# Kernel tuning notes

Hardware: AMD Instinct MI355X
Metric: run time of the kernel (lower is better)

## Reference

```python
import jax, jax.numpy as jnp
import numpy as np

N = 50000      # total nodes in batched graph
E = 800000     # total edges
G = 512        # number of graphs in the batch
NF = 32        # input node feature dim
EF = 16        # edge feature dim
HID = [64, 128, 128, 256]


def _seg_mean(vals, ids, num):
    s = jax.ops.segment_sum(vals, ids, num_segments=num)
    c = jax.ops.segment_sum(jnp.ones((vals.shape[0], 1), vals.dtype), ids, num_segments=num)
    return s / jnp.maximum(c, 1.0)


def setup_inputs() -> dict:
    key = jax.random.key(0)
    ks = list(jax.random.split(key, 64))
    it = iter(ks)

    def nk():
        return next(it)

    inp = {}
    inp["x"] = jax.random.normal(nk(), (N, NF), jnp.float32)
    inp["e"] = jax.random.normal(nk(), (E, EF), jnp.float32)
    inp["src"] = jax.random.randint(nk(), (E,), 0, N)
    inp["dst"] = jax.random.randint(nk(), (E,), 0, N)
    inp["gid"] = jnp.sort(jax.random.randint(nk(), (N,), 0, G))
    fin = NF
    for i, f in enumerate(HID):
        inp[f"Wm{i}"] = jax.random.normal(nk(), (fin + EF, f), jnp.float32) / np.sqrt(fin + EF)
        inp[f"bm{i}"] = jnp.zeros((f,), jnp.float32)
        inp[f"Ws{i}"] = jax.random.normal(nk(), (fin, f), jnp.float32) / np.sqrt(fin)
        inp[f"bs{i}"] = jnp.zeros((f,), jnp.float32)
        inp[f"Wc{i}"] = jax.random.normal(nk(), (f, 1), jnp.float32) / np.sqrt(f)
        inp[f"bc{i}"] = jnp.zeros((1,), jnp.float32)
        fin = f
    return inp


def _molconv(x, e, src, dst, Wm, bm, Ws, bs):
    # gather source node feats, condition on edge feats, per-edge MLP
    m = jax.nn.relu(jnp.concatenate([x[src], e], axis=-1) @ Wm + bm)  # [E, out]
    agg = _seg_mean(m, dst, x.shape[0])                               # scatter-mean to dst
    return jax.nn.relu(agg + x @ Ws + bs)                             # [N, out]


def reference(x, e, src, dst, gid,
              Wm0, bm0, Ws0, bs0, Wc0, bc0,
              Wm1, bm1, Ws1, bs1, Wc1, bc1,
              Wm2, bm2, Ws2, bs2, Wc2, bc2,
              Wm3, bm3, Ws3, bs3, Wc3, bc3):
    layers = [(Wm0, bm0, Ws0, bs0, Wc0, bc0),
              (Wm1, bm1, Ws1, bs1, Wc1, bc1),
              (Wm2, bm2, Ws2, bs2, Wc2, bc2),
              (Wm3, bm3, Ws3, bs3, Wc3, bc3)]
    feat = x
    score = jnp.zeros((G, 1), x.dtype)
    for Wm, bm, Ws, bs, Wc, bc in layers:
        feat = _molconv(feat, e, src, dst, Wm, bm, Ws, bs)
        # per-layer Linear(feats,1) classifier + AvgPooling per graph, summed
        score = score + _seg_mean(feat @ Wc + bc, gid, G)
    return score
```

## Files before the change

kernel.cpp:

```cpp
#include <hip/hip_runtime.h>

#define NN 50000
#define EE 800000
#define GG 512
#define NP 50048
#define EB 3125
#define SCB 196

typedef short bf16x8 __attribute__((ext_vector_type(8)));
typedef float floatx4 __attribute__((ext_vector_type(4)));

__device__ inline unsigned short f2b(float f) {
    unsigned u = __float_as_uint(f);
    unsigned r = (u + 0x7fffu + ((u >> 16) & 1u)) >> 16;
    return (unsigned short)r;
}
__device__ inline float b2f(unsigned short b) {
    return __uint_as_float(((unsigned)b) << 16);
}


__global__ void conv_all(const float* __restrict__ x, unsigned short* __restrict__ xb, long n8x,
                         const float* __restrict__ ef, unsigned short* __restrict__ efB, long n8e) {
    long i = (long)blockIdx.x * blockDim.x + threadIdx.x;
    const float* s;
    unsigned short* d;
    long idx;
    if (i < n8x) { s = x; d = xb; idx = i; }
    else if (i < n8x + n8e) { s = ef; d = efB; idx = i - n8x; }
    else return;
    float4 a = ((const float4*)s)[2 * idx];
    float4 b = ((const float4*)s)[2 * idx + 1];
    unsigned short o[8] = {f2b(a.x), f2b(a.y), f2b(a.z), f2b(a.w),
                           f2b(b.x), f2b(b.y), f2b(b.z), f2b(b.w)};
    ((uint4*)d)[idx] = *(uint4*)o;
}


struct TpD { const float* W; unsigned short* WT; int K, F, Kp, rowOff; };
struct TpTab { TpD d[12]; };

__global__ void tp_all(TpTab t) {
    TpD dd = t.d[blockIdx.y];
    int f = blockIdx.x;
    if (f >= dd.F) return;
    for (int k = threadIdx.x; k < dd.Kp; k += blockDim.x)
        dd.WT[(size_t)f * dd.Kp + k] =
            (k < dd.K) ? f2b(dd.W[(size_t)(dd.rowOff + k) * dd.F + f]) : (unsigned short)0;
}


__global__ void hist_cnt(const int* __restrict__ dst, int* __restrict__ hist,
                         const int* __restrict__ gid, float* __restrict__ gcnt) {
    int b = blockIdx.x;
    if (b < EB) {
        int e = b * 256 + threadIdx.x;
        if (e < EE) atomicAdd(&hist[dst[e]], 1);
    } else {
        int n = (b - EB) * 256 + threadIdx.x;
        if (n < NN) atomicAdd(&gcnt[gid[n]], 1.0f);
    }
}

__global__ void scanA(const int* __restrict__ hist, int* __restrict__ bsum) {
    __shared__ int sb[256];
    int idx = blockIdx.x * 256 + threadIdx.x;
    sb[threadIdx.x] = (idx < NN) ? hist[idx] : 0;
    __syncthreads();
    for (int off = 128; off > 0; off >>= 1) {
        if (threadIdx.x < off) sb[threadIdx.x] += sb[threadIdx.x + off];
        __syncthreads();
    }
    if (threadIdx.x == 0) bsum[blockIdx.x] = sb[0];
}

__global__ void scanB(const int* __restrict__ bsum, int* __restrict__ boff) {
    __shared__ int sb[256];
    int t = threadIdx.x;
    int v = (t < SCB) ? bsum[t] : 0;
    sb[t] = v;
    __syncthreads();
    for (int off = 1; off < 256; off <<= 1) {
        int u = (t >= off) ? sb[t - off] : 0;
        __syncthreads();
        sb[t] += u;
        __syncthreads();
    }
    if (t < SCB) boff[t] = sb[t] - v;
}

__global__ void scanC(const int* __restrict__ hist, const int* __restrict__ boff,
                      int* __restrict__ cursor, float* __restrict__ invdeg,
                      float* __restrict__ gcnt, float* __restrict__ score,
                      const float* __restrict__ bc0, const float* __restrict__ bc1,
                      const float* __restrict__ bc2, const float* __restrict__ bc3) {
    __shared__ int sb[256];
    int t = threadIdx.x;
    int idx = blockIdx.x * 256 + t;
    int v = (idx < NN) ? hist[idx] : 0;
    sb[t] = v;
    __syncthreads();
    for (int off = 1; off < 256; off <<= 1) {
        int u = (t >= off) ? sb[t - off] : 0;
        __syncthreads();
        sb[t] += u;
        __syncthreads();
    }
    if (idx < NN) {
        cursor[idx] = boff[blockIdx.x] + sb[t] - v;
        invdeg[idx] = 1.0f / fmaxf((float)v, 1.0f);
    }
    if (idx < GG) {
        float c = gcnt[idx];
        gcnt[idx] = 1.0f / fmaxf(c, 1.0f);
        score[idx] = (c > 0.0f) ? (bc0[0] + bc1[0] + bc2[0] + bc3[0]) : 0.0f;
    }
}

__global__ void scatter_kernel(const int* __restrict__ src, const int* __restrict__ dst,
                               int* __restrict__ cursor, const unsigned short* __restrict__ efB,
                               int* __restrict__ srcS, int* __restrict__ dstS,
                               unsigned short* __restrict__ efS) {
    int e = blockIdx.x * blockDim.x + threadIdx.x;
    if (e < EE) {
        int d = dst[e];
        int p = atomicAdd(&cursor[d], 1);
        srcS[p] = src[e];
        dstS[p] = d;
        const uint4* s = (const uint4*)&efB[(size_t)e * 16];
        uint4* dd = (uint4*)&efS[(size_t)p * 16];
        dd[0] = s[0];
        dd[1] = s[1];
    }
}


template<int FIN, int F>
__global__ __launch_bounds__(256)
void nodeP(const unsigned short* __restrict__ featB, const unsigned short* __restrict__ WxT,
           unsigned short* __restrict__ P, float* __restrict__ agg)
{
    const int tid = threadIdx.x;
    const int w   = tid >> 6;
    const int l   = tid & 63;
    const int l16 = l & 15;
    const int q   = l >> 4;
    const int cb  = blockIdx.y * 64;
    const int nb  = blockIdx.x * 64;
    const int row = nb + w * 16 + l16;

    {
        const int zr = nb + (tid >> 4);
        const int zc = cb + ((tid & 15) << 2);
        const float4 z4 = {0.f, 0.f, 0.f, 0.f};
        #pragma unroll
        for (int i = 0; i < 4; ++i) {
            int n = zr + i * 16;
            if (n < NN) *(float4*)&agg[(size_t)n * F + zc] = z4;
        }
    }

    floatx4 acc[4];
    #pragma unroll
    for (int nt = 0; nt < 4; ++nt) acc[nt] = (floatx4){0.f, 0.f, 0.f, 0.f};

    #pragma unroll
    for (int kb = 0; kb < FIN; kb += 32) {
        bf16x8 a = *(const bf16x8*)&featB[(size_t)row * FIN + kb + q * 8];
        #pragma unroll
        for (int nt = 0; nt < 4; ++nt) {
            bf16x8 b = *(const bf16x8*)&WxT[(size_t)(cb + nt * 16 + l16) * FIN + kb + q * 8];
            acc[nt] = __builtin_amdgcn_mfma_f32_16x16x32_bf16(a, b, acc[nt], 0, 0, 0);
        }
    }

    #pragma unroll
    for (int nt = 0; nt < 4; ++nt)
        #pragma unroll
        for (int r = 0; r < 4; ++r) {
            int ro = nb + w * 16 + q * 4 + r;
            P[(size_t)ro * F + cb + nt * 16 + l16] = f2b(acc[nt][r]);
        }
}


#define RXO(r) ((((r) >> 2 & 1) << 4) | (((r) >> 3 & 1) << 3))

template<int F>
__global__ __launch_bounds__(256)
void edge_q(const unsigned short* __restrict__ efS,
            const int* __restrict__ srcS, const int* __restrict__ dstS,
            const unsigned short* __restrict__ WeT, const unsigned short* __restrict__ P,
            const float* __restrict__ bm, float* __restrict__ agg)
{
    constexpr int CW  = (F >= 128) ? 128 : 64;
    constexpr int WPG = F / CW;
    constexpr int NT  = CW / 16;
    constexpr int EPB = 64 * (4 / WPG);
    constexpr int RS  = CW;

    __shared__ __align__(16) float red[4][16 * RS];

    const int tid = threadIdx.x;
    const int w   = tid >> 6;
    const int l   = tid & 63;
    const int l16 = l & 15;
    const int q   = l >> 4;
    const int sub = w / WPG;
    const int cb  = (w % WPG) * CW;
    const int be  = blockIdx.x * EPB + sub * 64;

    const int dreg = dstS[be + l];
    const int sreg = srcS[be + l];

    const int dnext = __shfl_down(dreg, 1);
    const unsigned long long em = __ballot((l == 63) || (dreg != dnext));

    const bf16x8 ZV = {0, 0, 0, 0, 0, 0, 0, 0};
    const int xo = ((q & 1) << 4) | ((q >> 1) << 3);
    float* redw = &red[w][0];

    bf16x8 bfr[NT];
    #pragma unroll
    for (int nt = 0; nt < NT; ++nt)
        bfr[nt] = *(const bf16x8*)&WeT[(size_t)(cb + nt * 16 + l16) * 32 + q * 8];

    if constexpr (CW == 128) {
        float2 bmv;
        bmv.x = bm[cb + 2 * l];
        bmv.y = bm[cb + 2 * l + 1];

        float2 csum = {0.f, 0.f};
        bool first = true;

        #pragma unroll
        for (int mt = 0; mt < 4; ++mt) {
            bf16x8 a = ZV;
            if (q < 2) a = *(const bf16x8*)&efS[(size_t)(be + mt * 16 + l16) * 16 + q * 8];
            unsigned pvv[16];
            #pragma unroll
            for (int r = 0; r < 16; ++r) {
                int sr = __shfl(sreg, mt * 16 + r);
                pvv[r] = *(const unsigned*)&P[(size_t)sr * F + cb + 2 * l];
            }

            #pragma unroll
            for (int nt = 0; nt < NT; ++nt) {
                floatx4 acc = __builtin_amdgcn_mfma_f32_16x16x32_bf16(
                    a, bfr[nt], (floatx4){0.f, 0.f, 0.f, 0.f}, 0, 0, 0);
                #pragma unroll
                for (int r4 = 0; r4 < 4; ++r4)
                    redw[(q * 4 + r4) * RS + ((nt * 16 + l16) ^ xo)] = acc[r4];
            }

            #pragma unroll
            for (int r = 0; r < 16; ++r) {
                const int gr = mt * 16 + r;
                float2 qv = *(const float2*)&redw[r * RS + ((2 * l) ^ RXO(r))];
                csum.x += fmaxf(qv.x + __uint_as_float(pvv[r] << 16)          + bmv.x, 0.f);
                csum.y += fmaxf(qv.y + __uint_as_float(pvv[r] & 0xffff0000u) + bmv.y, 0.f);
                if ((em >> gr) & 1ull) {
                    int d = __shfl(dreg, gr);
                    float* ap = &agg[(size_t)d * F + cb + 2 * l];
                    if (first || gr == 63) { atomicAdd(ap, csum.x); atomicAdd(ap + 1, csum.y); }
                    else                   { *(float2*)ap = csum; }
                    csum.x = 0.f; csum.y = 0.f;
                    first = false;
                }
            }
        }
    } else {
        const float bmv = bm[cb + l];

        float csum = 0.f;
        bool first = true;

        #pragma unroll
        for (int mt = 0; mt < 4; ++mt) {
            bf16x8 a = ZV;
            if (q < 2) a = *(const bf16x8*)&efS[(size_t)(be + mt * 16 + l16) * 16 + q * 8];
            float pvv[16];
            #pragma unroll
            for (int r = 0; r < 16; ++r) {
                int sr = __shfl(sreg, mt * 16 + r);
                pvv[r] = b2f(P[(size_t)sr * F + cb + l]);
            }

            #pragma unroll
            for (int nt = 0; nt < NT; ++nt) {
                floatx4 acc = __builtin_amdgcn_mfma_f32_16x16x32_bf16(
                    a, bfr[nt], (floatx4){0.f, 0.f, 0.f, 0.f}, 0, 0, 0);
                #pragma unroll
                for (int r4 = 0; r4 < 4; ++r4)
                    redw[(q * 4 + r4) * RS + ((nt * 16 + l16) ^ xo)] = acc[r4];
            }

            #pragma unroll
            for (int r = 0; r < 16; ++r) {
                const int gr = mt * 16 + r;
                float qv = redw[r * RS + (l ^ RXO(r))];
                csum += fmaxf(qv + pvv[r] + bmv, 0.f);
                if ((em >> gr) & 1ull) {
                    int d = __shfl(dreg, gr);
                    float* ap = &agg[(size_t)d * F + cb + l];
                    if (first || gr == 63) atomicAdd(ap, csum);
                    else                   *ap = csum;
                    csum = 0.f;
                    first = false;
                }
            }
        }
    }
}


template<int FIN, int F>
__global__ __launch_bounds__(256)
void node_mfma(const unsigned short* __restrict__ featB, const float* __restrict__ agg,
               const unsigned short* __restrict__ WsT, const float* __restrict__ bs,
               const float* __restrict__ Wc, const float* __restrict__ invdeg,
               unsigned short* __restrict__ fout, float* __restrict__ rd)
{
    const int tid = threadIdx.x;
    const int w   = tid >> 6;
    const int l   = tid & 63;
    const int l16 = l & 15;
    const int q   = l >> 4;
    const int cb  = blockIdx.y * 64;
    const int nb  = blockIdx.x * 64;
    const int row = nb + w * 16 + l16;

    floatx4 acc[4];
    #pragma unroll
    for (int nt = 0; nt < 4; ++nt) acc[nt] = (floatx4){0.f, 0.f, 0.f, 0.f};

    #pragma unroll
    for (int kb = 0; kb < FIN; kb += 32) {
        bf16x8 a = *(const bf16x8*)&featB[(size_t)row * FIN + kb + q * 8];
        #pragma unroll
        for (int nt = 0; nt < 4; ++nt) {
            bf16x8 b = *(const bf16x8*)&WsT[(size_t)(cb + nt * 16 + l16) * FIN + kb + q * 8];
            acc[nt] = __builtin_amdgcn_mfma_f32_16x16x32_bf16(a, b, acc[nt], 0, 0, 0);
        }
    }

    float wcv[4], bsv[4];
    #pragma unroll
    for (int nt = 0; nt < 4; ++nt) {
        wcv[nt] = Wc[cb + nt * 16 + l16];
        bsv[nt] = bs[cb + nt * 16 + l16];
    }

    #pragma unroll
    for (int r = 0; r < 4; ++r) {
        int n = nb + w * 16 + q * 4 + r;
        bool valid = n < NN;
        float idg = valid ? invdeg[n] : 0.f;
        float s = 0.f;
        #pragma unroll
        for (int nt = 0; nt < 4; ++nt) {
            int col = cb + nt * 16 + l16;
            float av = valid ? agg[(size_t)n * F + col] : 0.f;
            float v = fmaxf(acc[nt][r] + av * idg + bsv[nt], 0.f);
            if (valid) fout[(size_t)n * F + col] = f2b(v);
            s += v * wcv[nt];
        }
        s += __shfl_xor(s, 1);
        s += __shfl_xor(s, 2);
        s += __shfl_xor(s, 4);
        s += __shfl_xor(s, 8);
        if (valid && l16 == 0) atomicAdd(&rd[n], s);
    }
}


__global__ void score_reduce(const float* __restrict__ rd, const int* __restrict__ gid,
                             const float* __restrict__ invg, float* __restrict__ score) {
    int n = blockIdx.x * blockDim.x + threadIdx.x;
    int l = threadIdx.x & 63;
    bool valid = n < NN;
    int g = valid ? gid[n] : -1;
    float v = valid ? rd[n] : 0.f;
    #pragma unroll
    for (int off = 1; off < 64; off <<= 1) {
        float vo = __shfl_up(v, off);
        int go = __shfl_up(g, off);
        if (l >= off && go == g) v += vo;
    }
    int gn = __shfl_down(g, 1);
    bool tail = (l == 63) || (gn != g);
    if (valid && tail) atomicAdd(&score[g], v * invg[g]);
}


extern "C" void kernel_launch(void* const* d_in, const int* in_sizes, int n_in,
                              void* d_out, int out_size, void* d_ws, size_t ws_size,
                              hipStream_t stream) {
    const float* x   = (const float*)d_in[0];
    const float* ef  = (const float*)d_in[1];
    const int*   src = (const int*)d_in[2];
    const int*   dst = (const int*)d_in[3];
    const int*   gid = (const int*)d_in[4];
    const float *Wm[4], *bm[4], *Ws[4], *bs[4], *Wc[4], *bc[4];
    for (int i = 0; i < 4; ++i) {
        Wm[i] = (const float*)d_in[5 + 6 * i];
        bm[i] = (const float*)d_in[6 + 6 * i];
        Ws[i] = (const float*)d_in[7 + 6 * i];
        bs[i] = (const float*)d_in[8 + 6 * i];
        Wc[i] = (const float*)d_in[9 + 6 * i];
        bc[i] = (const float*)d_in[10 + 6 * i];
    }

    char* w = (char*)d_ws;
    float* agg = (float*)w;                  w += (size_t)NN * 256 * 4;
    unsigned short* xb  = (unsigned short*)w; w += (size_t)NP * 32 * 2;
    unsigned short* f1  = (unsigned short*)w; w += (size_t)NP * 64 * 2;
    unsigned short* f2  = (unsigned short*)w; w += (size_t)NP * 128 * 2;
    unsigned short* f3  = (unsigned short*)w; w += (size_t)NP * 128 * 2;
    unsigned short* f4  = (unsigned short*)w; w += (size_t)NP * 256 * 2;
    unsigned short* P   = (unsigned short*)w; w += (size_t)NP * 256 * 2;
    unsigned short* efB = (unsigned short*)w; w += (size_t)EE * 16 * 2;
    unsigned short* efS = (unsigned short*)w; w += (size_t)EE * 16 * 2;
    unsigned short* WxT0 = (unsigned short*)w; w += (size_t)64 * 32 * 2;
    unsigned short* WxT1 = (unsigned short*)w; w += (size_t)128 * 64 * 2;
    unsigned short* WxT2 = (unsigned short*)w; w += (size_t)128 * 128 * 2;
    unsigned short* WxT3 = (unsigned short*)w; w += (size_t)256 * 128 * 2;
    unsigned short* WeT0 = (unsigned short*)w; w += (size_t)64 * 32 * 2;
    unsigned short* WeT1 = (unsigned short*)w; w += (size_t)128 * 32 * 2;
    unsigned short* WeT2 = (unsigned short*)w; w += (size_t)128 * 32 * 2;
    unsigned short* WeT3 = (unsigned short*)w; w += (size_t)256 * 32 * 2;
    unsigned short* WsT0 = (unsigned short*)w; w += (size_t)64 * 32 * 2;
    unsigned short* WsT1 = (unsigned short*)w; w += (size_t)128 * 64 * 2;
    unsigned short* WsT2 = (unsigned short*)w; w += (size_t)128 * 128 * 2;
    unsigned short* WsT3 = (unsigned short*)w; w += (size_t)256 * 128 * 2;
    float* invdeg = (float*)w;               w += (size_t)NN * 4;
    float* invg   = (float*)w;               w += (size_t)GG * 4;
    float* rd     = (float*)w;               w += (size_t)NN * 4;
    int* hist   = (int*)w;                   w += (size_t)(NN + 1) * 4;
    int* srcS   = (int*)w;                   w += (size_t)EE * 4;
    int* dstS   = (int*)w;                   w += (size_t)EE * 4;
    int* bsum   = (int*)w;                   w += (size_t)SCB * 4;
    int* boff   = (int*)w;                   w += (size_t)SCB * 4;
    int* cursor = (int*)w;                   w += (size_t)NN * 4;
    float* score = (float*)d_out;

    const long n8x = (long)NN * 32 / 8, n8e = (long)EE * 16 / 8;
    conv_all<<<(n8x + n8e + 255) / 256, 256, 0, stream>>>(x, xb, n8x, ef, efB, n8e);

    TpTab tt;
    tt.d[0]  = {Wm[0], WxT0,  32,  64,  32,   0};
    tt.d[1]  = {Wm[1], WxT1,  64, 128,  64,   0};
    tt.d[2]  = {Wm[2], WxT2, 128, 128, 128,   0};
    tt.d[3]  = {Wm[3], WxT3, 128, 256, 128,   0};
    tt.d[4]  = {Wm[0], WeT0,  16,  64,  32,  32};
    tt.d[5]  = {Wm[1], WeT1,  16, 128,  32,  64};
    tt.d[6]  = {Wm[2], WeT2,  16, 128,  32, 128};
    tt.d[7]  = {Wm[3], WeT3,  16, 256,  32, 128};
    tt.d[8]  = {Ws[0], WsT0,  32,  64,  32,   0};
    tt.d[9]  = {Ws[1], WsT1,  64, 128,  64,   0};
    tt.d[10] = {Ws[2], WsT2, 128, 128, 128,   0};
    tt.d[11] = {Ws[3], WsT3, 128, 256, 128,   0};
    tp_all<<<dim3(256, 12), 256, 0, stream>>>(tt);

    hipMemsetAsync(invg, 0, (size_t)(GG + NN + NN + 1) * 4, stream);
    hist_cnt<<<EB + SCB, 256, 0, stream>>>(dst, hist, gid, invg);
    scanA<<<SCB, 256, 0, stream>>>(hist, bsum);
    scanB<<<1, 256, 0, stream>>>(bsum, boff);
    scanC<<<SCB, 256, 0, stream>>>(hist, boff, cursor, invdeg, invg, score,
                                   bc[0], bc[1], bc[2], bc[3]);
    scatter_kernel<<<EB, 256, 0, stream>>>(src, dst, cursor, efB, srcS, dstS, efS);

    const int NB = NP / 64;

    nodeP<32, 64><<<dim3(NB, 1), 256, 0, stream>>>(xb, WxT0, P, agg);
    edge_q<64><<<EB, 256, 0, stream>>>(efS, srcS, dstS, WeT0, P, bm[0], agg);
    node_mfma<32, 64><<<dim3(NB, 1), 256, 0, stream>>>(xb, agg, WsT0, bs[0], Wc[0], invdeg, f1, rd);

    nodeP<64, 128><<<dim3(NB, 2), 256, 0, stream>>>(f1, WxT1, P, agg);
    edge_q<128><<<EB, 256, 0, stream>>>(efS, srcS, dstS, WeT1, P, bm[1], agg);
    node_mfma<64, 128><<<dim3(NB, 2), 256, 0, stream>>>(f1, agg, WsT1, bs[1], Wc[1], invdeg, f2, rd);

    nodeP<128, 128><<<dim3(NB, 2), 256, 0, stream>>>(f2, WxT2, P, agg);
    edge_q<128><<<EB, 256, 0, stream>>>(efS, srcS, dstS, WeT2, P, bm[2], agg);
    node_mfma<128, 128><<<dim3(NB, 2), 256, 0, stream>>>(f2, agg, WsT2, bs[2], Wc[2], invdeg, f3, rd);

    nodeP<128, 256><<<dim3(NB, 4), 256, 0, stream>>>(f3, WxT3, P, agg);
    edge_q<256><<<EE / 128, 256, 0, stream>>>(efS, srcS, dstS, WeT3, P, bm[3], agg);
    node_mfma<128, 256><<<dim3(NB, 4), 256, 0, stream>>>(f3, agg, WsT3, bs[3], Wc[3], invdeg, f4, rd);

    score_reduce<<<SCB, 256, 0, stream>>>(rd, gid, invg, score);
}
```

Measured before the change: 665.5 us.

## Store edge aggregation buffer in bf16 with packed bf16 atomics, fold bias into MFMA

The per-destination aggregation buffer moves from fp32 to bf16. Edge kernels write packed bf16 pairs and use global_atomic_pk_add_bf16 at segment boundaries, and the node kernel reads bf16. This halves the traffic for zeroing, scattering and re-reading agg. The edge-MLP bias is now passed as the MFMA accumulator initial value, which removes a per-element add. The cost is lower accumulation precision for the partial-sum atomics and an extra shuffle in the F=64 path to pair adjacent lanes.

New measurement: 642.7 us. 3.4% less time.

```diff
diff --git a/kernel.cpp b/kernel.cpp
--- a/kernel.cpp
+++ b/kernel.cpp
@@ -17,6 +17,13 @@
 }
 __device__ inline float b2f(unsigned short b) {
     return __uint_as_float(((unsigned)b) << 16);
+}
+__device__ inline unsigned pk2(float x, float y) {
+    return (unsigned)f2b(x) | ((unsigned)f2b(y) << 16);
+}
+__device__ inline void atomic_pk(unsigned short* p, unsigned v) {
+    asm volatile("global_atomic_pk_add_bf16 %0, %1, off"
+                 :: "v"(p), "v"(v) : "memory");
 }
 
 
@@ -138,7 +145,7 @@
 template<int FIN, int F>
 __global__ __launch_bounds__(256)
 void nodeP(const unsigned short* __restrict__ featB, const unsigned short* __restrict__ WxT,
-           unsigned short* __restrict__ P, float* __restrict__ agg)
+           unsigned short* __restrict__ P, unsigned short* __restrict__ agg)
 {
     const int tid = threadIdx.x;
     const int w   = tid >> 6;
@@ -150,13 +157,12 @@
     const int row = nb + w * 16 + l16;
 
     {
-        const int zr = nb + (tid >> 4);
-        const int zc = cb + ((tid & 15) << 2);
-        const float4 z4 = {0.f, 0.f, 0.f, 0.f};
-        #pragma unroll
-        for (int i = 0; i < 4; ++i) {
-            int n = zr + i * 16;
-            if (n < NN) *(float4*)&agg[(size_t)n * F + zc] = z4;
+        const int zr = nb + (tid >> 2);
+        const int zc = cb + ((tid & 3) << 4);
+        if (zr < NN) {
+            const uint4 z4 = {0u, 0u, 0u, 0u};
+            *(uint4*)&agg[(size_t)zr * F + zc]     = z4;
+            *(uint4*)&agg[(size_t)zr * F + zc + 8] = z4;
         }
     }
 
@@ -191,7 +197,7 @@
 void edge_q(const unsigned short* __restrict__ efS,
             const int* __restrict__ srcS, const int* __restrict__ dstS,
             const unsigned short* __restrict__ WeT, const unsigned short* __restrict__ P,
-            const float* __restrict__ bm, float* __restrict__ agg)
+            const float* __restrict__ bm, unsigned short* __restrict__ agg)
 {
     constexpr int CW  = (F >= 128) ? 128 : 64;
     constexpr int WPG = F / CW;
@@ -221,15 +227,14 @@
     float* redw = &red[w][0];
 
     bf16x8 bfr[NT];
-    #pragma unroll
-    for (int nt = 0; nt < NT; ++nt)
+    float  bmc[NT];
+    #pragma unroll
+    for (int nt = 0; nt < NT; ++nt) {
         bfr[nt] = *(const bf16x8*)&WeT[(size_t)(cb + nt * 16 + l16) * 32 + q * 8];
+        bmc[nt] = bm[cb + nt * 16 + l16];
+    }
 
     if constexpr (CW == 128) {
-        float2 bmv;
-        bmv.x = bm[cb + 2 * l];
-        bmv.y = bm[cb + 2 * l + 1];
-
         float2 csum = {0.f, 0.f};
         bool first = true;
 
@@ -247,7 +252,7 @@
             #pragma unroll
             for (int nt = 0; nt < NT; ++nt) {
                 floatx4 acc = __builtin_amdgcn_mfma_f32_16x16x32_bf16(
-                    a, bfr[nt], (floatx4){0.f, 0.f, 0.f, 0.f}, 0, 0, 0);
+                    a, bfr[nt], (floatx4){bmc[nt], bmc[nt], bmc[nt], bmc[nt]}, 0, 0, 0);
                 #pragma unroll
                 for (int r4 = 0; r4 < 4; ++r4)
                     redw[(q * 4 + r4) * RS + ((nt * 16 + l16) ^ xo)] = acc[r4];
@@ -257,21 +262,20 @@
             for (int r = 0; r < 16; ++r) {
                 const int gr = mt * 16 + r;
                 float2 qv = *(const float2*)&redw[r * RS + ((2 * l) ^ RXO(r))];
-                csum.x += fmaxf(qv.x + __uint_as_float(pvv[r] << 16)          + bmv.x, 0.f);
-                csum.y += fmaxf(qv.y + __uint_as_float(pvv[r] & 0xffff0000u) + bmv.y, 0.f);
+                csum.x += fmaxf(qv.x + __uint_as_float(pvv[r] << 16), 0.f);
+                csum.y += fmaxf(qv.y + __uint_as_float(pvv[r] & 0xffff0000u), 0.f);
                 if ((em >> gr) & 1ull) {
                     int d = __shfl(dreg, gr);
-                    float* ap = &agg[(size_t)d * F + cb + 2 * l];
-                    if (first || gr == 63) { atomicAdd(ap, csum.x); atomicAdd(ap + 1, csum.y); }
-                    else                   { *(float2*)ap = csum; }
+                    unsigned short* ap = &agg[(size_t)d * F + cb + 2 * l];
+                    unsigned pv = pk2(csum.x, csum.y);
+                    if (first || gr == 63) atomic_pk(ap, pv);
+                    else                   *(unsigned*)ap = pv;
                     csum.x = 0.f; csum.y = 0.f;
                     first = false;
                 }
             }
         }
     } else {
-        const float bmv = bm[cb + l];
-
         float csum = 0.f;
         bool first = true;
 
@@ -289,7 +293,7 @@
             #pragma unroll
             for (int nt = 0; nt < NT; ++nt) {
                 floatx4 acc = __builtin_amdgcn_mfma_f32_16x16x32_bf16(
-                    a, bfr[nt], (floatx4){0.f, 0.f, 0.f, 0.f}, 0, 0, 0);
+                    a, bfr[nt], (floatx4){bmc[nt], bmc[nt], bmc[nt], bmc[nt]}, 0, 0, 0);
                 #pragma unroll
                 for (int r4 = 0; r4 < 4; ++r4)
                     redw[(q * 4 + r4) * RS + ((nt * 16 + l16) ^ xo)] = acc[r4];
@@ -299,12 +303,16 @@
             for (int r = 0; r < 16; ++r) {
                 const int gr = mt * 16 + r;
                 float qv = redw[r * RS + (l ^ RXO(r))];
-                csum += fmaxf(qv + pvv[r] + bmv, 0.f);
+                csum += fmaxf(qv + pvv[r], 0.f);
                 if ((em >> gr) & 1ull) {
                     int d = __shfl(dreg, gr);
-                    float* ap = &agg[(size_t)d * F + cb + l];
-                    if (first || gr == 63) atomicAdd(ap, csum);
-                    else                   *ap = csum;
+                    float cn = __shfl_down(csum, 1);
+                    if ((l & 1) == 0) {
+                        unsigned short* ap = &agg[(size_t)d * F + cb + l];
+                        unsigned pv = pk2(csum, cn);
+                        if (first || gr == 63) atomic_pk(ap, pv);
+                        else                   *(unsigned*)ap = pv;
+                    }
                     csum = 0.f;
                     first = false;
                 }
@@ -316,7 +324,7 @@
 
 template<int FIN, int F>
 __global__ __launch_bounds__(256)
-void node_mfma(const unsigned short* __restrict__ featB, const float* __restrict__ agg,
+void node_mfma(const unsigned short* __restrict__ featB, const unsigned short* __restrict__ agg,
                const unsigned short* __restrict__ WsT, const float* __restrict__ bs,
                const float* __restrict__ Wc, const float* __restrict__ invdeg,
                unsigned short* __restrict__ fout, float* __restrict__ rd)
@@ -360,7 +368,7 @@
         #pragma unroll
         for (int nt = 0; nt < 4; ++nt) {
             int col = cb + nt * 16 + l16;
-            float av = valid ? agg[(size_t)n * F + col] : 0.f;
+            float av = valid ? b2f(agg[(size_t)n * F + col]) : 0.f;
             float v = fmaxf(acc[nt][r] + av * idg + bsv[nt], 0.f);
             if (valid) fout[(size_t)n * F + col] = f2b(v);
             s += v * wcv[nt];
@@ -412,7 +420,7 @@
     }
 
     char* w = (char*)d_ws;
-    float* agg = (float*)w;                  w += (size_t)NN * 256 * 4;
+    unsigned short* agg = (unsigned short*)w;  w += (size_t)NN * 256 * 4;
     unsigned short* xb  = (unsigned short*)w; w += (size_t)NP * 32 * 2;
     unsigned short* f1  = (unsigned short*)w; w += (size_t)NP * 64 * 2;
     unsigned short* f2  = (unsigned short*)w; w += (size_t)NP * 128 * 2;
```
